# Performance work log

Hardware: AMD Instinct MI355X
Metric: run time of the kernel (lower is better)

## Reference

```python
import jax, jax.numpy as jnp
import numpy as np
import math

HEAD_NUM = 16


def _split_qkv(qkv, head_num):
    # torch: rearrange(qkv, 'b t (d k h) -> k b h t d', k=3, h=head_num)
    B, T, E3 = qkv.shape
    d = E3 // (3 * head_num)
    qkv = qkv.reshape(B, T, d, 3, head_num)        # (b,t,d,k,h)
    qkv = jnp.transpose(qkv, (3, 0, 4, 1, 2))       # (k,b,h,t,d)
    return qkv[0], qkv[1], qkv[2]


def setup_inputs() -> dict:
    key = jax.random.key(0)
    ks = jax.random.split(key, 6)
    B, T, E = 4, 1024, 1024
    return {
        "x": jax.random.normal(ks[0], (B, T, E), dtype=jnp.float32),
        "y": jax.random.normal(ks[1], (B, T, E), dtype=jnp.float32),
        "Wqkv1": jax.random.normal(ks[2], (3 * E, E), dtype=jnp.float32) * 0.02,
        "Wqkv2": jax.random.normal(ks[3], (3 * E, E), dtype=jnp.float32) * 0.02,
        "Wout1": jax.random.normal(ks[4], (E, E), dtype=jnp.float32) * 0.02,
        "Wout2": jax.random.normal(ks[5], (E, E), dtype=jnp.float32) * 0.02,
    }


def reference(x, y, Wqkv1, Wqkv2, Wout1, Wout2):
    B, T, E = x.shape
    H = HEAD_NUM
    dk = math.sqrt(E / H)

    qkv1 = x @ Wqkv1.T                              # (B,T,3E)
    qkv2 = y @ Wqkv2.T
    q1, k1, v1 = _split_qkv(qkv1, H)                # each (B,H,T,d)
    q2, k2, v2 = _split_qkv(qkv2, H)

    # cross attention: stream-2 queries attend to stream-1 keys/values and vice versa
    energy1 = jnp.einsum('bhid,bhjd->bhij', q2, k1) / dk
    energy2 = jnp.einsum('bhid,bhjd->bhij', q1, k2) / dk
    attn1 = jax.nn.softmax(energy1, axis=-1)
    attn2 = jax.nn.softmax(energy2, axis=-1)

    xo = jnp.einsum('bhij,bhjd->bhid', attn1, v1)   # (B,H,T,d)
    yo = jnp.einsum('bhij,bhjd->bhid', attn2, v2)
    xo = jnp.transpose(xo, (0, 2, 1, 3)).reshape(B, T, E)  # b t (h d)
    yo = jnp.transpose(yo, (0, 2, 1, 3)).reshape(B, T, E)

    return xo @ Wout1.T, yo @ Wout2.T
```

## Files before the change

### kernel.cpp

```cpp
#include <hip/hip_runtime.h>
#include <hip/hip_bf16.h>

typedef __hip_bfloat16 bf16;
typedef __attribute__((ext_vector_type(8))) short short8;
typedef __attribute__((ext_vector_type(4))) short short4v;
typedef __attribute__((ext_vector_type(4))) float f32x4;

#define MFMA_BF16(a, b, c) __builtin_amdgcn_mfma_f32_16x16x32_bf16((a), (b), (c), 0, 0, 0)

#define QSCALE 0.1803368860111270f

__device__ __forceinline__ short f2bf(float f) {
    union { bf16 h; short s; } u;
    u.h = __float2bfloat16(f);
    return u.s;
}

#if defined(__has_builtin) && __has_builtin(__builtin_amdgcn_cvt_pk_bf16_f32)
typedef __attribute__((ext_vector_type(2))) __bf16 bf16x2_t;
__device__ __forceinline__ unsigned int pk2(float a, float b) {
    union { bf16x2_t v; unsigned int u; } x;
    x.v = __builtin_amdgcn_cvt_pk_bf16_f32(a, b);
    return x.u;
}
#else
__device__ __forceinline__ unsigned int pk2(float a, float b) {
    union { bf16 h[2]; unsigned int u; } x;
    x.h[0] = __float2bfloat16(a);
    x.h[1] = __float2bfloat16(b);
    return x.u;
}
#endif

#if defined(__has_builtin) && __has_builtin(__builtin_amdgcn_exp2f)
#define EXP2F(x) __builtin_amdgcn_exp2f(x)
#else
#define EXP2F(x) exp2f(x)
#endif

__device__ __forceinline__ void gload16(const void* g, void* l) {
    __builtin_amdgcn_global_load_lds(
        (const __attribute__((address_space(1))) unsigned int*)g,
        (__attribute__((address_space(3))) unsigned int*)l, 16, 0, 0);
}

__global__ void cvt_fused(const float* __restrict__ x, const float* __restrict__ y,
                          const float* __restrict__ wo1, const float* __restrict__ wo2,
                          const float* __restrict__ wq1, const float* __restrict__ wq2,
                          bf16* __restrict__ ox, bf16* __restrict__ oy,
                          bf16* __restrict__ oo1, bf16* __restrict__ oo2,
                          bf16* __restrict__ oq1, bf16* __restrict__ oq2) {
    const int yb = blockIdx.y;
    if (yb < 4) {
        int i = blockIdx.x * 256 + threadIdx.x;
        const float* src; bf16* dst; int n4;
        switch (yb) {
            case 0:  src = x;   dst = ox;  n4 = 1048576; break;
            case 1:  src = y;   dst = oy;  n4 = 1048576; break;
            case 2:  src = wo1; dst = oo1; n4 = 262144;  break;
            default: src = wo2; dst = oo2; n4 = 262144;  break;
        }
        if (i >= n4) return;
        float4 f = reinterpret_cast<const float4*>(src)[i];
        short4v s;
        s.x = f2bf(f.x); s.y = f2bf(f.y); s.z = f2bf(f.z); s.w = f2bf(f.w);
        reinterpret_cast<short4v*>(dst)[i] = s;
    } else {
        const int np = blockIdx.x;
        if (np >= 3072) return;
        const int comp = np >> 10, rem = np & 1023, h = rem >> 6, d = rem & 63;
        const int srow = d * 48 + comp * 16 + h;
        const float* src = ((yb == 5) ? wq2 : wq1) + (long)srow * 1024;
        bf16* dst = ((yb == 5) ? oq2 : oq1) + (long)np * 1024;
        const float sc = (comp == 0) ? QSCALE : 1.0f;
        int t = threadIdx.x;
        float4 f = reinterpret_cast<const float4*>(src)[t];
        short4v s;
        s.x = f2bf(f.x * sc); s.y = f2bf(f.y * sc); s.z = f2bf(f.z * sc); s.w = f2bf(f.w * sc);
        reinterpret_cast<short4v*>(dst)[t] = s;
    }
}

__global__ __launch_bounds__(512, 2)
void gemm_qkv128(const bf16* __restrict__ A0g, const bf16* __restrict__ B0g,
                 void* o0a, void* o0b, void* o0c,
                 const bf16* __restrict__ A1g, const bf16* __restrict__ B1g,
                 void* o1a, void* o1b, void* o1c) {
    extern __shared__ short smem[];
    const int z = blockIdx.z;
    const short* A = reinterpret_cast<const short*>(z ? A1g : A0g);
    const short* B = reinterpret_cast<const short*>(z ? B1g : B0g);
    const int tid  = threadIdx.x;
    const int lane = tid & 63;
    const int w    = tid >> 6;
    const int quad = lane >> 4;
    const int l16  = lane & 15;
    const long M0 = (long)blockIdx.y * 128;
    const long N0 = (long)blockIdx.x * 256;

    const int wm = w >> 2;
    const int wn = w & 3;
    const int cA0  = (quad ^ (l16 & 7)) * 8;
    const int aoff = wm * 4096 + l16 * 64;
    const int boff = 8192 + wn * 2048 + l16 * 64;
    const int w512 = w * 512;

    const short* Asrc = A + (M0 + w * 8 + (lane >> 3)) * 1024 + ((lane & 7) ^ (lane >> 3)) * 8;
    const short* Bsrc = B + (N0 + w * 8 + (lane >> 3)) * 1024 + ((lane & 7) ^ (lane >> 3)) * 8;

    f32x4 acc[2][4][2] = {};
    short8 af[4][2], bfv[2][2];

#define SA128(tt, nbase) do { \
    const short* _s = Asrc + (tt) * 64; \
    short* _d = smem + (nbase) + w512; \
    gload16(_s, _d); gload16(_s + 65536, _d + 4096); } while (0)
#define SB128(half, tt, nbase) do { \
    const short* _s = Bsrc + (half) * 131072 + (tt) * 64; \
    short* _d = smem + (nbase) + 8192 + (half) * 8192 + w512; \
    gload16(_s, _d); gload16(_s + 65536, _d + 4096); } while (0)
#define RDA128(bbv) do { \
    _Pragma("unroll") for (int mt = 0; mt < 4; ++mt) { \
        const short* _p = &smem[(bbv) + aoff + mt * 1024]; \
        af[mt][0] = *reinterpret_cast<const short8*>(_p + cA0); \
        af[mt][1] = *reinterpret_cast<const short8*>(_p + (cA0 ^ 32)); } } while (0)
#define RDB128(Bh, bbv) do { \
    _Pragma("unroll") for (int nt = 0; nt < 2; ++nt) { \
        const short* _p = &smem[(bbv) + (Bh) * 8192 + boff + nt * 1024]; \
        bfv[nt][0] = *reinterpret_cast<const short8*>(_p + cA0); \
        bfv[nt][1] = *reinterpret_cast<const short8*>(_p + (cA0 ^ 32)); } } while (0)
#define MM128(p) do { \
    __builtin_amdgcn_s_setprio(1); \
    _Pragma("unroll") for (int mt = 0; mt < 4; ++mt) \
    _Pragma("unroll") for (int nt = 0; nt < 2; ++nt) { \
        acc[p][mt][nt] = MFMA_BF16(af[mt][0], bfv[nt][0], acc[p][mt][nt]); \
        acc[p][mt][nt] = MFMA_BF16(af[mt][1], bfv[nt][1], acc[p][mt][nt]); } \
    __builtin_amdgcn_s_setprio(0); } while (0)

    SA128(0, 0); SB128(0, 0, 0); SB128(1, 0, 0);

    int bcur = 0;
#pragma unroll 1
    for (int t = 0; t < 16; ++t) {
        int bnext = bcur + 1; if (bnext == 3) bnext = 0;
        if (t < 15) {
            const int nb = bnext * 24576;
            SA128(t + 1, nb); SB128(0, t + 1, nb); SB128(1, t + 1, nb);
            asm volatile("s_waitcnt vmcnt(6)" ::: "memory");
        } else {
            asm volatile("s_waitcnt vmcnt(0)" ::: "memory");
        }
        __builtin_amdgcn_s_barrier();
        __builtin_amdgcn_sched_barrier(0);

        const int bb = bcur * 24576;
        RDA128(bb);
        RDB128(0, bb);
        MM128(0);
        RDB128(1, bb);
        MM128(1);
        bcur = bnext;
    }

    __syncthreads();

    if (blockIdx.x < 8) {
        short* dst = reinterpret_cast<short*>(blockIdx.x < 4 ? (z ? o1a : o0a)
                                                             : (z ? o1b : o0b));
        const int b = (int)(M0 >> 10);
        const int t00 = ((int)M0 & 1023) + wm * 64 + quad * 4;
        const int hd00 = ((int)blockIdx.x & 3) * 256 + wn * 32;
#pragma unroll
        for (int Bh = 0; Bh < 2; ++Bh)
#pragma unroll
            for (int nt = 0; nt < 2; ++nt) {
                const int hd = hd00 + Bh * 128 + nt * 16 + l16;
                const int h = hd >> 6, d = hd & 63;
                short* dp = dst + (long)(b * 16 + h) * 65536 + d;
#pragma unroll
                for (int mt = 0; mt < 4; ++mt)
#pragma unroll
                    for (int r = 0; r < 4; ++r)
                        dp[(long)(t00 + mt * 16 + r) * 64] = f2bf(acc[Bh][mt][nt][r]);
            }
    } else {
        short* vT = reinterpret_cast<short*>(z ? o1c : o0c);
        const int b = (int)(M0 >> 10);
        const int hd00 = ((int)blockIdx.x - 8) * 256 + wn * 32;
        short* ws = smem + w * 2304;
        const int c8 = (lane & 7) * 8;
        const int colr = lane >> 3;
        const int tb = ((int)M0 & 1023) + wm * 64 + c8;
#pragma unroll
        for (int Bh = 0; Bh < 2; ++Bh) {
#pragma unroll
            for (int nt = 0; nt < 2; ++nt)
#pragma unroll
                for (int mt = 0; mt < 4; ++mt) {
                    uint2 uu;
                    uu.x = pk2(acc[Bh][mt][nt][0], acc[Bh][mt][nt][1]);
                    uu.y = pk2(acc[Bh][mt][nt][2], acc[Bh][mt][nt][3]);
                    *reinterpret_cast<uint2*>(&ws[(nt * 16 + l16) * 72 + mt * 16 + quad * 4]) = uu;
                }
#pragma unroll
            for (int q4 = 0; q4 < 4; ++q4) {
                const int col = q4 * 8 + colr;
                const int hd = hd00 + Bh * 128 + col;
                const int h = hd >> 6, d = hd & 63;
                short8 v = *reinterpret_cast<const short8*>(&ws[col * 72 + c8]);
                *reinterpret_cast<short8*>(&vT[(long)(b * 16 + h) * 65536 + (long)d * 1024 + tb]) = v;
            }
        }
    }
#undef SA128
#undef SB128
#undef RDA128
#undef RDB128
#undef MM128
}

__global__ __launch_bounds__(256)
void gemm_out(const bf16* __restrict__ A0g, const bf16* __restrict__ B0g, float* __restrict__ C0,
              const bf16* __restrict__ A1g, const bf16* __restrict__ B1g, float* __restrict__ C1) {
    __shared__ short smem2[24576];
    const int z = blockIdx.z;
    const short* A = reinterpret_cast<const short*>(z ? A1g : A0g);
    const short* B = reinterpret_cast<const short*>(z ? B1g : B0g);
    const int tid  = threadIdx.x;
    const int lane = tid & 63;
    const int w    = tid >> 6;
    const int wr   = w >> 1;
    const int wc   = w & 1;
    const int quad = lane >> 4;
    const int l16  = lane & 15;
    const long bM = (long)blockIdx.y * 128;

    f32x4 acc[4][4] = {};

    const int sr  = lane >> 2;
    const int scs = ((lane & 3) ^ (sr & 3)) * 8;
    const short* Ag0 = A + (bM + 32 * w + sr) * 1024 + scs;
    const short* Ag1 = Ag0 + 16 * 1024;
    const short* Bg0 = B + ((long)blockIdx.x * 128 + 32 * w + sr) * 1024 + scs;
    const short* Bg1 = Bg0 + 16 * 1024;
    const int sq = (quad ^ (l16 & 3)) * 8;

    {
        short* sb = smem2;
        gload16(Ag0, sb + w * 1024);
        gload16(Ag1, sb + w * 1024 + 512);
        gload16(Bg0, sb + 4096 + w * 1024);
        gload16(Bg1, sb + 4096 + w * 1024 + 512);
    }

    int bcur = 0;
#pragma unroll 1
    for (int iter = 0; iter < 32; ++iter) {
        int bnext = bcur + 1; if (bnext == 3) bnext = 0;
        if (iter < 31) {
            const int koff = (iter + 1) * 32;
            short* sb = smem2 + bnext * 8192;
            gload16(Ag0 + koff, sb + w * 1024);
            gload16(Ag1 + koff, sb + w * 1024 + 512);
            gload16(Bg0 + koff, sb + 4096 + w * 1024);
            gload16(Bg1 + koff, sb + 4096 + w * 1024 + 512);
            asm volatile("s_waitcnt vmcnt(4)" ::: "memory");
        } else {
            asm volatile("s_waitcnt vmcnt(0)" ::: "memory");
        }
        __builtin_amdgcn_s_barrier();
        __builtin_amdgcn_sched_barrier(0);

        const short* Ab = smem2 + bcur * 8192;
        const short* Bb = Ab + 4096;

        short8 af[4], bfr[4];
#pragma unroll
        for (int mt = 0; mt < 4; ++mt)
            af[mt] = *reinterpret_cast<const short8*>(&Ab[(wr * 64 + mt * 16 + l16) * 32 + sq]);
#pragma unroll
        for (int nt = 0; nt < 4; ++nt)
            bfr[nt] = *reinterpret_cast<const short8*>(&Bb[(wc * 64 + nt * 16 + l16) * 32 + sq]);
        __builtin_amdgcn_s_setprio(1);
#pragma unroll
        for (int mt = 0; mt < 4; ++mt)
#pragma unroll
            for (int nt = 0; nt < 4; ++nt)
                acc[mt][nt] = MFMA_BF16(af[mt], bfr[nt], acc[mt][nt]);
        __builtin_amdgcn_s_setprio(0);
        bcur = bnext;
    }

    float* C = z ? C1 : C0;
    const long crow = bM + wr * 64 + quad * 4;
    const long ccol = (long)blockIdx.x * 128 + wc * 64 + l16;
#pragma unroll
    for (int mt = 0; mt < 4; ++mt)
#pragma unroll
        for (int nt = 0; nt < 4; ++nt)
#pragma unroll
            for (int r = 0; r < 4; ++r)
                C[(crow + mt * 16 + r) * 1024L + ccol + nt * 16] = acc[mt][nt][r];
}

__global__ __launch_bounds__(256)
void attn_kernel(const bf16* __restrict__ q0g, const bf16* __restrict__ k0g,
                 const bf16* __restrict__ v0g, bf16* __restrict__ o0g,
                 const bf16* __restrict__ q1g, const bf16* __restrict__ k1g,
                 const bf16* __restrict__ v1g, bf16* __restrict__ o1g) {
    __shared__ short smem[24576];
    const int bh = blockIdx.x;
    const int qt = blockIdx.y;
    const int z = blockIdx.z;
    const int b = bh >> 4, h = bh & 15;
    const int tid = threadIdx.x, lane = tid & 63, w = tid >> 6;
    const int quad = lane >> 4, l16 = lane & 15;

    const short* Qb = reinterpret_cast<const short*>(z ? q1g : q0g) + (long)bh * 1024 * 64;
    const short* Kb = reinterpret_cast<const short*>(z ? k1g : k0g) + (long)bh * 1024 * 64;
    const short* Vb = reinterpret_cast<const short*>(z ? v1g : v0g) + (long)bh * 64 * 1024;
    short* Ob = reinterpret_cast<short*>(z ? o1g : o0g);

    short8 qb[2][2];
#pragma unroll
    for (int qg = 0; qg < 2; ++qg) {
        const short* Qp = Qb + (long)(qt * 128 + qg * 64 + w * 16 + l16) * 64;
        qb[qg][0] = *reinterpret_cast<const short8*>(Qp + quad * 8);
        qb[qg][1] = *reinterpret_cast<const short8*>(Qp + 32 + quad * 8);
    }

    const int r8  = lane >> 3;
    const int sc0 = ((lane & 7) ^ (r8 & 3)) * 8;
    const short* Kg0 = Kb + (long)(16 * w + r8) * 64 + sc0;
    const short* Kg1 = Kb + (long)(16 * w + 8 + r8) * 64 + (sc0 ^ 32);
    const short* Vg0 = Vb + (long)(16 * w + r8) * 1024 + sc0;
    const short* Vg1 = Vb + (long)(16 * w + 8 + r8) * 1024 + (sc0 ^ 32);

    const int jbase = 8 * (l16 >> 2) + (l16 & 3);
    const int fKs = (l16 & 3) | (((l16 >> 2) & 1) << 2);
    const int s0  = (quad ^ fKs) * 8;
    const int fVs = (l16 & 3) | (((l16 >> 3) & 1) << 2);
    const int sv  = (quad ^ fVs) * 8;

    f32x4 o[2][4] = {};
    float li[2] = {0.f, 0.f};

    gload16(Kg0, smem + w * 1024); gload16(Kg1, smem + w * 1024 + 512);
    gload16(Vg0, smem + 4096 + w * 1024); gload16(Vg1, smem + 4096 + w * 1024 + 512);

    int bcur = 0;
#pragma unroll 1
    for (int iter = 0; iter < 16; ++iter) {
        int bnext = bcur + 1; if (bnext == 3) bnext = 0;
        if (iter < 15) {
            short* sb = smem + bnext * 8192;
            const long ko = (long)(iter + 1) * 4096;
            const long vo = (long)(iter + 1) * 64;
            gload16(Kg0 + ko, sb + w * 1024);
            gload16(Kg1 + ko, sb + w * 1024 + 512);
            gload16(Vg0 + vo, sb + 4096 + w * 1024);
            gload16(Vg1 + vo, sb + 4096 + w * 1024 + 512);
            asm volatile("s_waitcnt vmcnt(4)" ::: "memory");
        } else {
            asm volatile("s_waitcnt vmcnt(0)" ::: "memory");
        }
        __builtin_amdgcn_s_barrier();
        __builtin_amdgcn_sched_barrier(0);

        const short* Ks = smem + bcur * 8192;
        const short* Vs = Ks + 4096;

        f32x4 st[2][4];
        __builtin_amdgcn_s_setprio(1);
#pragma unroll
        for (int g = 0; g < 4; ++g) {
            const int goff = (g >> 1) * 32 + (g & 1) * 4;
            const short* kr = Ks + (jbase + goff) * 64;
            short8 k0 = *reinterpret_cast<const short8*>(kr + s0);
            short8 k1 = *reinterpret_cast<const short8*>(kr + (s0 ^ 32));
#pragma unroll
            for (int qg = 0; qg < 2; ++qg) {
                f32x4 zf = {0.f, 0.f, 0.f, 0.f};
                zf = MFMA_BF16(k0, qb[qg][0], zf);
                zf = MFMA_BF16(k1, qb[qg][1], zf);
                st[qg][g] = zf;
            }
        }
        __builtin_amdgcn_s_setprio(0);

        union { unsigned int u[4]; short8 s; } f0[2], f1[2];
#pragma unroll
        for (int qg = 0; qg < 2; ++qg) {
            float p[4][4];
            float rs = 0.f;
#pragma unroll
            for (int g = 0; g < 4; ++g)
#pragma unroll
                for (int r = 0; r < 4; ++r) {
                    float e = EXP2F(st[qg][g][r]);
                    p[g][r] = e;
                    rs += e;
                }
            li[qg] += rs;
            f0[qg].u[0] = pk2(p[0][0], p[0][1]); f0[qg].u[1] = pk2(p[0][2], p[0][3]);
            f0[qg].u[2] = pk2(p[1][0], p[1][1]); f0[qg].u[3] = pk2(p[1][2], p[1][3]);
            f1[qg].u[0] = pk2(p[2][0], p[2][1]); f1[qg].u[1] = pk2(p[2][2], p[2][3]);
            f1[qg].u[2] = pk2(p[3][0], p[3][1]); f1[qg].u[3] = pk2(p[3][2], p[3][3]);
        }

        __builtin_amdgcn_s_setprio(1);
#pragma unroll
        for (int dt = 0; dt < 4; ++dt) {
            const short* vr = Vs + (dt * 16 + l16) * 64;
            short8 v0 = *reinterpret_cast<const short8*>(vr + sv);
            short8 v1 = *reinterpret_cast<const short8*>(vr + (sv ^ 32));
#pragma unroll
            for (int qg = 0; qg < 2; ++qg) {
                o[qg][dt] = MFMA_BF16(v0, f0[qg].s, o[qg][dt]);
                o[qg][dt] = MFMA_BF16(v1, f1[qg].s, o[qg][dt]);
            }
        }
        __builtin_amdgcn_s_setprio(0);
        bcur = bnext;
    }

    __syncthreads();

#pragma unroll
    for (int qg = 0; qg < 2; ++qg) {
        li[qg] += __shfl_xor(li[qg], 16);
        li[qg] += __shfl_xor(li[qg], 32);
    }

#pragma unroll
    for (int qg = 0; qg < 2; ++qg) {
        short* Os = smem + qg * 5120 + w * 1280;
        const float rl = 1.0f / li[qg];
#pragma unroll
        for (int dt = 0; dt < 4; ++dt) {
            uint2 uu;
            uu.x = pk2(o[qg][dt][0] * rl, o[qg][dt][1] * rl);
            uu.y = pk2(o[qg][dt][2] * rl, o[qg][dt][3] * rl);
            *reinterpret_cast<uint2*>(&Os[l16 * 80 + dt * 16 + quad * 4]) = uu;
        }
#pragma unroll
        for (int p = 0; p < 2; ++p) {
            int row = p * 8 + (lane >> 3);
            int ch = (lane & 7) * 8;
            short8 v = *reinterpret_cast<const short8*>(&Os[row * 80 + ch]);
            *reinterpret_cast<short8*>(&Ob[((long)(b * 1024) + qt * 128 + qg * 64 + w * 16 + row) * 1024 + h * 64 + ch]) = v;
        }
    }
}

extern "C" void kernel_launch(void* const* d_in, const int* in_sizes, int n_in,
                              void* d_out, int out_size, void* d_ws, size_t ws_size,
                              hipStream_t stream) {
    const float* x     = (const float*)d_in[0];
    const float* y     = (const float*)d_in[1];
    const float* Wqkv1 = (const float*)d_in[2];
    const float* Wqkv2 = (const float*)d_in[3];
    const float* Wout1 = (const float*)d_in[4];
    const float* Wout2 = (const float*)d_in[5];

    char* ws = (char*)d_ws;
    bf16* Wqkv1b = (bf16*)(ws + 0);
    bf16* Wqkv2b = (bf16*)(ws + 6291456);
    bf16* Wout1b = (bf16*)(ws + 12582912);
    bf16* Wout2b = (bf16*)(ws + 14680064);
    bf16* xb     = (bf16*)(ws + 16777216);
    bf16* yb     = (bf16*)(ws + 25165824);
    bf16* q1     = (bf16*)(ws + 33554432);
    bf16* k1     = (bf16*)(ws + 41943040);
    bf16* v1T    = (bf16*)(ws + 50331648);
    bf16* q2     = (bf16*)(ws + 58720256);
    bf16* k2     = (bf16*)(ws + 67108864);
    bf16* v2T    = (bf16*)(ws + 75497472);
    bf16* xo     = xb;
    bf16* yo     = yb;

    static bool s_attr = false;
    if (!s_attr) {
        (void)hipFuncSetAttribute(reinterpret_cast<const void*>(&gemm_qkv128),
                                  hipFuncAttributeMaxDynamicSharedMemorySize, 147456);
        s_attr = true;
    }

    cvt_fused<<<dim3(4096, 6), 256, 0, stream>>>(x, y, Wout1, Wout2, Wqkv1, Wqkv2,
                                                 xb, yb, Wout1b, Wout2b, Wqkv1b, Wqkv2b);

    gemm_qkv128<<<dim3(12, 32, 2), 512, 147456, stream>>>(xb, Wqkv1b, q1, k1, v1T,
                                                          yb, Wqkv2b, q2, k2, v2T);

    attn_kernel<<<dim3(64, 8, 2), 256, 0, stream>>>(q2, k1, v1T, xo,
                                                    q1, k2, v2T, yo);

    gemm_out<<<dim3(8, 32, 2), 256, 0, stream>>>(xo, Wout1b, (float*)d_out,
                                                 yo, Wout2b, ((float*)d_out) + 4194304);
}
```

Before: 237.9 us.

## Halve QKV GEMM K-tile to 32 to double occupancy and cut LDS

The QKV projection GEMM now stages K-slices of 32 instead of 64. This halves the triple-buffered shared-memory footprint to 72KB and the fragment registers, and raises the launch-bounds occupancy hint from 2 to 4 blocks. The swizzle, load mapping and waitcnt counts are reworked to match, and the main loop runs 32 iterations instead of 16. The aim is more resident waves to hide memory latency, at the cost of twice as many barriers and less work per iteration to amortize them.

```diff
diff --git a/kernel.cpp b/kernel.cpp
--- a/kernel.cpp
+++ b/kernel.cpp
@@ -81,7 +81,7 @@
     }
 }
 
-__global__ __launch_bounds__(512, 2)
+__global__ __launch_bounds__(512, 4)
 void gemm_qkv128(const bf16* __restrict__ A0g, const bf16* __restrict__ B0g,
                  void* o0a, void* o0b, void* o0c,
                  const bf16* __restrict__ A1g, const bf16* __restrict__ B1g,
@@ -100,60 +100,54 @@
 
     const int wm = w >> 2;
     const int wn = w & 3;
-    const int cA0  = (quad ^ (l16 & 7)) * 8;
-    const int aoff = wm * 4096 + l16 * 64;
-    const int boff = 8192 + wn * 2048 + l16 * 64;
-    const int w512 = w * 512;
-
-    const short* Asrc = A + (M0 + w * 8 + (lane >> 3)) * 1024 + ((lane & 7) ^ (lane >> 3)) * 8;
-    const short* Bsrc = B + (N0 + w * 8 + (lane >> 3)) * 1024 + ((lane & 7) ^ (lane >> 3)) * 8;
+    const int cA0  = (quad ^ (l16 & 3)) * 8;
+    const int aoff = wm * 2048 + l16 * 32;
+    const int boff = 4096 + wn * 1024 + l16 * 32;
+
+    const int srow = lane >> 2;
+    const int scs  = ((lane & 3) ^ (srow & 3)) * 8;
+    const short* Asrc = A + (M0 + 16 * w + srow) * 1024 + scs;
+    const short* Bsrc = B + (N0 + 32 * w + srow) * 1024 + scs;
 
     f32x4 acc[2][4][2] = {};
-    short8 af[4][2], bfv[2][2];
+    short8 af[4], bfv[2];
 
 #define SA128(tt, nbase) do { \
-    const short* _s = Asrc + (tt) * 64; \
-    short* _d = smem + (nbase) + w512; \
-    gload16(_s, _d); gload16(_s + 65536, _d + 4096); } while (0)
-#define SB128(half, tt, nbase) do { \
-    const short* _s = Bsrc + (half) * 131072 + (tt) * 64; \
-    short* _d = smem + (nbase) + 8192 + (half) * 8192 + w512; \
-    gload16(_s, _d); gload16(_s + 65536, _d + 4096); } while (0)
+    gload16(Asrc + (tt) * 32, smem + (nbase) + w * 512); } while (0)
+#define SB128(tt, nbase) do { \
+    const short* _s = Bsrc + (tt) * 32; \
+    short* _d = smem + (nbase) + 4096 + w * 1024; \
+    gload16(_s, _d); gload16(_s + 16384, _d + 512); } while (0)
 #define RDA128(bbv) do { \
-    _Pragma("unroll") for (int mt = 0; mt < 4; ++mt) { \
-        const short* _p = &smem[(bbv) + aoff + mt * 1024]; \
-        af[mt][0] = *reinterpret_cast<const short8*>(_p + cA0); \
-        af[mt][1] = *reinterpret_cast<const short8*>(_p + (cA0 ^ 32)); } } while (0)
+    _Pragma("unroll") for (int mt = 0; mt < 4; ++mt) \
+        af[mt] = *reinterpret_cast<const short8*>(&smem[(bbv) + aoff + mt * 512 + cA0]); } while (0)
 #define RDB128(Bh, bbv) do { \
-    _Pragma("unroll") for (int nt = 0; nt < 2; ++nt) { \
-        const short* _p = &smem[(bbv) + (Bh) * 8192 + boff + nt * 1024]; \
-        bfv[nt][0] = *reinterpret_cast<const short8*>(_p + cA0); \
-        bfv[nt][1] = *reinterpret_cast<const short8*>(_p + (cA0 ^ 32)); } } while (0)
+    _Pragma("unroll") for (int nt = 0; nt < 2; ++nt) \
+        bfv[nt] = *reinterpret_cast<const short8*>(&smem[(bbv) + (Bh) * 4096 + boff + nt * 512 + cA0]); } while (0)
 #define MM128(p) do { \
     __builtin_amdgcn_s_setprio(1); \
     _Pragma("unroll") for (int mt = 0; mt < 4; ++mt) \
-    _Pragma("unroll") for (int nt = 0; nt < 2; ++nt) { \
-        acc[p][mt][nt] = MFMA_BF16(af[mt][0], bfv[nt][0], acc[p][mt][nt]); \
-        acc[p][mt][nt] = MFMA_BF16(af[mt][1], bfv[nt][1], acc[p][mt][nt]); } \
+    _Pragma("unroll") for (int nt = 0; nt < 2; ++nt) \
+        acc[p][mt][nt] = MFMA_BF16(af[mt], bfv[nt], acc[p][mt][nt]); \
     __builtin_amdgcn_s_setprio(0); } while (0)
 
-    SA128(0, 0); SB128(0, 0, 0); SB128(1, 0, 0);
+    SA128(0, 0); SB128(0, 0);
 
     int bcur = 0;
 #pragma unroll 1
-    for (int t = 0; t < 16; ++t) {
+    for (int t = 0; t < 32; ++t) {
         int bnext = bcur + 1; if (bnext == 3) bnext = 0;
-        if (t < 15) {
-            const int nb = bnext * 24576;
-            SA128(t + 1, nb); SB128(0, t + 1, nb); SB128(1, t + 1, nb);
-            asm volatile("s_waitcnt vmcnt(6)" ::: "memory");
+        if (t < 31) {
+            const int nb = bnext * 12288;
+            SA128(t + 1, nb); SB128(t + 1, nb);
+            asm volatile("s_waitcnt vmcnt(3)" ::: "memory");
         } else {
             asm volatile("s_waitcnt vmcnt(0)" ::: "memory");
         }
         __builtin_amdgcn_s_barrier();
         __builtin_amdgcn_sched_barrier(0);
 
-        const int bb = bcur * 24576;
+        const int bb = bcur * 12288;
         RDA128(bb);
         RDB128(0, bb);
         MM128(0);
@@ -482,15 +476,15 @@
     static bool s_attr = false;
     if (!s_attr) {
         (void)hipFuncSetAttribute(reinterpret_cast<const void*>(&gemm_qkv128),
-                                  hipFuncAttributeMaxDynamicSharedMemorySize, 147456);
+                                  hipFuncAttributeMaxDynamicSharedMemorySize, 73728);
         s_attr = true;
     }
 
     cvt_fused<<<dim3(4096, 6), 256, 0, stream>>>(x, y, Wout1, Wout2, Wqkv1, Wqkv2,
                                                  xb, yb, Wout1b, Wout2b, Wqkv1b, Wqkv2b);
 
-    gemm_qkv128<<<dim3(12, 32, 2), 512, 147456, stream>>>(xb, Wqkv1b, q1, k1, v1T,
-                                                          yb, Wqkv2b, q2, k2, v2T);
+    gemm_qkv128<<<dim3(12, 32, 2), 512, 73728, stream>>>(xb, Wqkv1b, q1, k1, v1T,
+                                                         yb, Wqkv2b, q2, k2, v2T);
 
     attn_kernel<<<dim3(64, 8, 2), 256, 0, stream>>>(q2, k1, v1T, xo,
                                                     q1, k2, v2T, yo);
```

Result: no change. 240.1 us (+0.9%).
